# Performance work log

Hardware: AMD Instinct MI355X
Metric: run time of the kernel (lower is better)

The kernel has to match this reference:

```python
import jax, jax.numpy as jnp
import numpy as np

B, S, D_IN, H, NH, L = 8, 1024, 512, 1024, 16, 4
HD = H // NH
SCALE = HD ** -0.5
EPS = 1e-5


def _ln(x, g, b):
    m = jnp.mean(x, axis=-1, keepdims=True)
    v = jnp.mean((x - m) ** 2, axis=-1, keepdims=True)
    return (x - m) * jax.lax.rsqrt(v + EPS) * g + b


def setup_inputs() -> dict:
    key = jax.random.key(0)
    ks = jax.random.split(key, 12)
    s = lambda k, shape, fan: jax.random.normal(k, shape, jnp.float32) * (fan ** -0.5)
    return {
        "x": jax.random.normal(ks[0], (B, S, D_IN), jnp.float32),
        "W_in": s(ks[1], (D_IN, H), D_IN), "b_in": jnp.zeros((H,), jnp.float32),
        "W_qkv": s(ks[2], (L, H, 3 * H), H), "b_qkv": jnp.zeros((L, 3 * H), jnp.float32),
        "W_o": s(ks[3], (L, H, H), H), "b_o": jnp.zeros((L, H), jnp.float32),
        "g1": jnp.ones((L, H), jnp.float32), "be1": jnp.zeros((L, H), jnp.float32),
        "W_out": s(ks[4], (H, H), H), "b_out": jnp.zeros((H,), jnp.float32),
        "g2": jnp.ones((H,), jnp.float32), "be2": jnp.zeros((H,), jnp.float32),
    }


def _attn_layer(x, Wqkv, bqkv, Wo, bo, g, be):
    b, s, h = x.shape
    qkv = (x @ Wqkv + bqkv).reshape(b, s, 3, NH, HD)
    q = qkv[:, :, 0].transpose(0, 2, 1, 3)  # [B,NH,S,HD]
    k = qkv[:, :, 1].transpose(0, 2, 1, 3)
    v = qkv[:, :, 2].transpose(0, 2, 1, 3)
    scores = jnp.einsum("bhqd,bhkd->bhqk", q, k) * SCALE
    w = jax.nn.softmax(scores, axis=-1)  # dropout is identity in eval
    o = jnp.einsum("bhqk,bhkd->bhqd", w, v)
    o = o.transpose(0, 2, 1, 3).reshape(b, s, h)
    return _ln(o @ Wo + bo + x, g, be)


def reference(x, W_in, b_in, W_qkv, b_qkv, W_o, b_o, g1, be1, W_out, b_out, g2, be2):
    h = x @ W_in + b_in
    for i in range(L):
        h = _attn_layer(h, W_qkv[i], b_qkv[i], W_o[i], b_o[i], g1[i], be1[i])
    pooled = jnp.mean(h, axis=1)  # [B,H]
    return _ln(pooled @ W_out + b_out, g2, be2)
```

## Files before the change

kernel.cpp:

```cpp
#include <hip/hip_runtime.h>
#include <stdint.h>

typedef unsigned short u16;
typedef unsigned int   u32;
typedef __attribute__((ext_vector_type(8))) short short8;
typedef __attribute__((ext_vector_type(4))) float f32x4;

#define B_   8
#define S_   1024
#define DIN_ 512
#define H_   1024
#define NH_  16
#define HD_  64
#define L_   4
#define M_   (B_*S_)
#define SCALE_ 0.125f
#define EPS_ 1e-5f

__device__ __forceinline__ u16 f2b(float f) {
  u32 u = __builtin_bit_cast(u32, f);
  u32 r = (u + 0x7fffu + ((u >> 16) & 1u)) >> 16;
  return (u16)r;
}

__device__ __forceinline__ void gll16(const void* g, void* l) {
  __builtin_amdgcn_global_load_lds(
      (const __attribute__((address_space(1))) u32*)(uintptr_t)g,
      (__attribute__((address_space(3))) u32*)(uintptr_t)l,
      16, 0, 0);
}

__global__ void cvt_k(const float* __restrict__ in, u16* __restrict__ out) {
  long i = (long)(blockIdx.x * 256 + threadIdx.x) * 4;
  f32x4 v = *(const f32x4*)&in[i];
  u32 p0 = (u32)f2b(v[0]) | ((u32)f2b(v[1]) << 16);
  u32 p1 = (u32)f2b(v[2]) | ((u32)f2b(v[3]) << 16);
  u32* o = (u32*)&out[i];
  o[0] = p0; o[1] = p1;
}

__global__ __launch_bounds__(256)
void tcvt_k(const float* __restrict__ in0, u16* __restrict__ out0, int R, int C) {
  __shared__ float t[32][33];
  const float* in = in0 + (size_t)blockIdx.z * R * C;
  u16* out = out0 + (size_t)blockIdx.z * R * C;
  int tx = threadIdx.x & 31, ty = threadIdx.x >> 5;
  long r0 = blockIdx.y * 32, c0 = blockIdx.x * 32;
#pragma unroll
  for (int i = 0; i < 4; ++i)
    t[ty + i*8][tx] = in[(r0 + ty + i*8) * (long)C + c0 + tx];
  __syncthreads();
#pragma unroll
  for (int i = 0; i < 4; ++i)
    out[(c0 + ty + i*8) * (long)R + r0 + tx] = f2b(t[tx][ty + i*8]);
}

template<int EPI>
__global__ __launch_bounds__(256, 2)
void gemm_k(const u16* __restrict__ A, const u16* __restrict__ Bt,
            const float* __restrict__ bias,
            float* __restrict__ Cf, u16* __restrict__ Cb,
            const float* __restrict__ Res,
            int Ndim, int K, int scale_cols)
{
  __shared__ u16 As[128 * 32];
  __shared__ u16 Bs[128 * 32];
  const int tid = threadIdx.x;
  const int lane = tid & 63;
  const int wid = tid >> 6;
  const int wr = wid >> 1, wc = wid & 1;
  const int l15 = lane & 15, l4 = lane >> 4;
  const long arow0 = (long)blockIdx.x * 128;
  const long brow0 = (long)blockIdx.y * 128;

  f32x4 acc[4][4] = {};

  const int srow = tid >> 2;
  const int scol = (tid & 3) * 8;
  const u16* ga  = A  + (arow0 + srow) * K + scol;
  const u16* ga1 = ga + 64 * (long)K;
  const u16* gb  = Bt + (brow0 + srow) * K + scol;
  const u16* gb1 = gb + 64 * (long)K;
  u16* lA0 = &As[tid * 8];
  u16* lA1 = &As[2048 + tid * 8];
  u16* lB0 = &Bs[tid * 8];
  u16* lB1 = &Bs[2048 + tid * 8];

  for (int k0 = 0; k0 < K; k0 += 32) {
    gll16(ga + k0, lA0);
    gll16(ga1 + k0, lA1);
    gll16(gb + k0, lB0);
    gll16(gb1 + k0, lB1);
    __syncthreads();
    short8 af[4], bf[4];
#pragma unroll
    for (int m = 0; m < 4; ++m)
      af[m] = *(const short8*)&As[(wr*64 + m*16 + l15) * 32 + l4*8];
#pragma unroll
    for (int n = 0; n < 4; ++n)
      bf[n] = *(const short8*)&Bs[(wc*64 + n*16 + l15) * 32 + l4*8];
#pragma unroll
    for (int m = 0; m < 4; ++m)
#pragma unroll
      for (int n = 0; n < 4; ++n)
        acc[m][n] = __builtin_amdgcn_mfma_f32_16x16x32_bf16(af[m], bf[n], acc[m][n], 0, 0, 0);
    __syncthreads();
  }

  const int crow = wr*64 + l4*4;
  const int ccol = wc*64 + l15;
#pragma unroll
  for (int m = 0; m < 4; ++m) {
#pragma unroll
    for (int n = 0; n < 4; ++n) {
      const int col = (int)brow0 + ccol + n*16;
      const float bv = bias[col];
      const float sc = (EPI == 1 && col < scale_cols) ? SCALE_ : 1.0f;
#pragma unroll
      for (int r = 0; r < 4; ++r) {
        const long row = arow0 + crow + m*16 + r;
        float v = acc[m][n][r] + bv;
        if (EPI == 1) {
          Cb[row * Ndim + col] = f2b(v * sc);
        } else if (EPI == 0) {
          Cf[row * Ndim + col] = v;
          Cb[row * Ndim + col] = f2b(v);
        } else {
          Cf[row * Ndim + col] = v + Res[row * Ndim + col];
        }
      }
    }
  }
}

__global__ __launch_bounds__(256, 3)
void attn_k(const u16* __restrict__ qkv, u16* __restrict__ ob)
{
  __shared__ u16 Ks[2][4096];
  __shared__ u16 Vs[2][4096];
  __shared__ u16 Ps[4][2048];

  const int tid = threadIdx.x, lane = tid & 63, wid = tid >> 6;
  const int l15 = lane & 15, l4 = lane >> 4;

  const int hb = blockIdx.x;
  const int xcd = hb & 7, slot = hb >> 3;
  const int bh = xcd + ((slot >> 3) << 3);
  const int qx = slot & 7;
  const int b = bh >> 4, nh = bh & 15;
  const int q0 = qx * 128 + wid * 32;

  const int RS = 3 * H_;
  const long base = (long)b * S_ * RS;
  const u16* Qg = qkv + base + nh * HD_;
  const u16* Kg = qkv + base + H_ + nh * HD_;
  const u16* Vg = qkv + base + 2 * H_ + nh * HD_;

  short8 qf[2][2];
#pragma unroll
  for (int i = 0; i < 2; ++i)
#pragma unroll
    for (int kf = 0; kf < 2; ++kf)
      qf[i][kf] = *(const short8*)&Qg[(long)(q0 + i*16 + l15) * RS + kf*32 + l4*8];

  float m_[2] = {-1e30f, -1e30f};
  float l_[2] = {0.f, 0.f};
  f32x4 of[2][4] = {};

  const int vd = tid & 63;
  const int vk0 = (tid >> 6) * 8;
  const int vbyt0 = (vd*128 + (tid>>6)*16) ^ ((vd & 7) << 4);
  const int vbyt1 = (vd*128 + ((tid>>6)+4)*16) ^ ((vd & 7) << 4);

  {
#pragma unroll
    for (int i = 0; i < 2; ++i) {
      int c = (i*4 + wid) * 64 + lane;
      int row = c >> 3;
      int sc2 = (lane & 7) ^ (row & 7);
      gll16(Kg + (long)row * RS + sc2*8, (char*)&Ks[0][0] + (size_t)c*16);
    }
    union { u16 u[8]; short8 v; } ta, tb;
#pragma unroll
    for (int j = 0; j < 8; ++j) {
      ta.u[j] = Vg[(long)(vk0 + j) * RS + vd];
      tb.u[j] = Vg[(long)(vk0 + 32 + j) * RS + vd];
    }
    *(short8*)((char*)&Vs[0][0] + vbyt0) = ta.v;
    *(short8*)((char*)&Vs[0][0] + vbyt1) = tb.v;
  }
  __syncthreads();

  for (int t = 0; t < 16; ++t) {
    const int cur = t & 1, nxt = cur ^ 1;
    union { u16 u[8]; short8 v; } ta, tb;
    if (t < 15) {
      const int kv1 = (t + 1) * 64;
#pragma unroll
      for (int i = 0; i < 2; ++i) {
        int c = (i*4 + wid) * 64 + lane;
        int row = c >> 3;
        int sc2 = (lane & 7) ^ (row & 7);
        gll16(Kg + (long)(kv1 + row) * RS + sc2*8, (char*)&Ks[nxt][0] + (size_t)c*16);
      }
#pragma unroll
      for (int j = 0; j < 8; ++j) {
        ta.u[j] = Vg[(long)(kv1 + vk0 + j) * RS + vd];
        tb.u[j] = Vg[(long)(kv1 + vk0 + 32 + j) * RS + vd];
      }
    }

    f32x4 sv[2][4];
#pragma unroll
    for (int i = 0; i < 2; ++i)
#pragma unroll
      for (int f = 0; f < 4; ++f)
        sv[i][f] = (f32x4){0.f, 0.f, 0.f, 0.f};
    __builtin_amdgcn_s_setprio(1);
#pragma unroll
    for (int f = 0; f < 4; ++f) {
#pragma unroll
      for (int kf = 0; kf < 2; ++kf) {
        int krow = f*16 + l15;
        int kbyt = (krow*128 + (kf*32 + l4*8)*2) ^ ((krow & 7) << 4);
        short8 kfrag = *(const short8*)((const char*)&Ks[cur][0] + kbyt);
#pragma unroll
        for (int i = 0; i < 2; ++i)
          sv[i][f] = __builtin_amdgcn_mfma_f32_16x16x32_bf16(kfrag, qf[i][kf], sv[i][f], 0, 0, 0);
      }
    }
    __builtin_amdgcn_s_setprio(0);

#pragma unroll
    for (int i = 0; i < 2; ++i) {
      float tmax = -1e30f;
#pragma unroll
      for (int f = 0; f < 4; ++f)
#pragma unroll
        for (int r = 0; r < 4; ++r) tmax = fmaxf(tmax, sv[i][f][r]);
      tmax = fmaxf(tmax, __shfl_xor(tmax, 16));
      tmax = fmaxf(tmax, __shfl_xor(tmax, 32));
      const float mnew = fmaxf(m_[i], tmax);
      const float corr = __expf(m_[i] - mnew);
      float tsum = 0.f;
#pragma unroll
      for (int f = 0; f < 4; ++f) {
#pragma unroll
        for (int r = 0; r < 4; ++r) {
          float p = __expf(sv[i][f][r] - mnew);
          sv[i][f][r] = p;
          tsum += p;
        }
      }
      tsum += __shfl_xor(tsum, 16);
      tsum += __shfl_xor(tsum, 32);
      l_[i] = l_[i] * corr + tsum;
      m_[i] = mnew;
#pragma unroll
      for (int f = 0; f < 4; ++f) {
        u32 lo = (u32)f2b(sv[i][f][0]) | ((u32)f2b(sv[i][f][1]) << 16);
        u32 hi = (u32)f2b(sv[i][f][2]) | ((u32)f2b(sv[i][f][3]) << 16);
        int prow = i*16 + l15;
        int pbyt = (prow*128 + (f*16 + l4*4)*2) ^ ((prow & 7) << 4);
        u32* dst = (u32*)((char*)&Ps[wid][0] + pbyt);
        dst[0] = lo; dst[1] = hi;
      }
#pragma unroll
      for (int r = 0; r < 4; ++r) {
        float cr = __shfl(corr, (lane & 48) | (l4*4 + r));
#pragma unroll
        for (int nf = 0; nf < 4; ++nf) of[i][nf][r] *= cr;
      }
    }
    asm volatile("s_waitcnt lgkmcnt(0)" ::: "memory");
    __builtin_amdgcn_sched_barrier(0);

    __builtin_amdgcn_s_setprio(1);
#pragma unroll
    for (int kf = 0; kf < 2; ++kf) {
      short8 vf_[4];
#pragma unroll
      for (int nf = 0; nf < 4; ++nf) {
        int vrow = nf*16 + l15;
        int vbyt = (vrow*128 + (kf*32 + l4*8)*2) ^ ((vrow & 7) << 4);
        vf_[nf] = *(const short8*)((const char*)&Vs[cur][0] + vbyt);
      }
#pragma unroll
      for (int i = 0; i < 2; ++i) {
        int prow = i*16 + l15;
        int pbyt = (prow*128 + (kf*32 + l4*8)*2) ^ ((prow & 7) << 4);
        short8 pfrag = *(const short8*)((const char*)&Ps[wid][0] + pbyt);
#pragma unroll
        for (int nf = 0; nf < 4; ++nf)
          of[i][nf] = __builtin_amdgcn_mfma_f32_16x16x32_bf16(pfrag, vf_[nf], of[i][nf], 0, 0, 0);
      }
    }
    __builtin_amdgcn_s_setprio(0);

    if (t < 15) {
      *(short8*)((char*)&Vs[nxt][0] + vbyt0) = ta.v;
      *(short8*)((char*)&Vs[nxt][0] + vbyt1) = tb.v;
      __syncthreads();
    }
  }

#pragma unroll
  for (int i = 0; i < 2; ++i) {
#pragma unroll
    for (int r = 0; r < 4; ++r) {
      float li = __shfl(l_[i], (lane & 48) | (l4*4 + r));
      float inv = 1.0f / li;
      long srow = (long)(b * S_ + q0 + i*16 + l4*4 + r);
#pragma unroll
      for (int nf = 0; nf < 4; ++nf)
        ob[srow * H_ + nh*HD_ + nf*16 + l15] = f2b(of[i][nf][r] * inv);
    }
  }
}

__global__ __launch_bounds__(256)
void ln_k(const float* __restrict__ in, const float* __restrict__ g,
          const float* __restrict__ be, float* __restrict__ outf,
          u16* __restrict__ outb)
{
  const int row = blockIdx.x;
  const int tid = threadIdx.x;
  const float* x = in + (long)row * H_;
  f32x4 v = *(const f32x4*)&x[tid * 4];
  float s  = v[0] + v[1] + v[2] + v[3];
  float ss = v[0]*v[0] + v[1]*v[1] + v[2]*v[2] + v[3]*v[3];
#pragma unroll
  for (int o = 1; o < 64; o <<= 1) {
    s  += __shfl_xor(s, o);
    ss += __shfl_xor(ss, o);
  }
  __shared__ float rs[4], rq[4];
  const int wid = tid >> 6;
  if ((tid & 63) == 0) { rs[wid] = s; rq[wid] = ss; }
  __syncthreads();
  float ts = rs[0] + rs[1] + rs[2] + rs[3];
  float tq = rq[0] + rq[1] + rq[2] + rq[3];
  const float mu = ts * (1.0f / H_);
  const float var = tq * (1.0f / H_) - mu * mu;
  const float rstd = rsqrtf(var + EPS_);
  const long obase = (long)row * H_ + tid * 4;
#pragma unroll
  for (int j = 0; j < 4; ++j) {
    int c = tid * 4 + j;
    float y = (v[j] - mu) * rstd * g[c] + be[c];
    outf[obase + j] = y;
    if (outb) outb[obase + j] = f2b(y);
  }
}

__global__ void pool_k(const float* __restrict__ hf, float* __restrict__ pooled) {
  const int c = blockIdx.x * 256 + threadIdx.x;
  const int b = blockIdx.y;
  const int s0 = blockIdx.z * 128;
  float s = 0.f;
  for (int t = 0; t < 128; ++t) s += hf[((long)(b * S_ + s0 + t)) * H_ + c];
  atomicAdd(&pooled[b * H_ + c], s * (1.0f / S_));
}

__global__ void fgemm_k(const float* __restrict__ pooled, const float* __restrict__ W,
                        const float* __restrict__ bias, float* __restrict__ out) {
  const int n = blockIdx.x * 256 + threadIdx.x;
  const int b = blockIdx.y;
  float s = bias[n];
  for (int k = 0; k < H_; ++k) s += pooled[b * H_ + k] * W[(long)k * H_ + n];
  out[b * H_ + n] = s;
}

extern "C" void kernel_launch(void* const* d_in, const int* in_sizes, int n_in,
                              void* d_out, int out_size, void* d_ws, size_t ws_size,
                              hipStream_t stream) {
  const float* x     = (const float*)d_in[0];
  const float* W_in  = (const float*)d_in[1];
  const float* b_in  = (const float*)d_in[2];
  const float* W_qkv = (const float*)d_in[3];
  const float* b_qkv = (const float*)d_in[4];
  const float* W_o   = (const float*)d_in[5];
  const float* b_o   = (const float*)d_in[6];
  const float* g1    = (const float*)d_in[7];
  const float* be1   = (const float*)d_in[8];
  const float* W_out = (const float*)d_in[9];
  const float* b_out = (const float*)d_in[10];
  const float* g2    = (const float*)d_in[11];
  const float* be2   = (const float*)d_in[12];
  float* outp = (float*)d_out;

  char* ws = (char*)d_ws;
  float* hf    = (float*)(ws + 0);
  u16*   hb    = (u16*)(ws + 33554432);
  u16*   qkvb  = (u16*)(ws + 50331648);
  float* resf  = (float*)(ws + 50331648);
  u16*   ob    = (u16*)(ws + 100663296);
  u16*   xb    = (u16*)(ws + 100663296);
  u16*   WinT  = (u16*)(ws + 117440512);
  u16*   WqkvT = (u16*)(ws + 118489088);
  u16*   WoT   = (u16*)(ws + 143654912);
  float* pooled= (float*)(ws + 152043520);
  float* tmpf  = (float*)(ws + 152076288);

  cvt_k<<<dim3(M_ * DIN_ / 1024), 256, 0, stream>>>(x, xb);
  tcvt_k<<<dim3(H_/32, DIN_/32, 1), 256, 0, stream>>>(W_in, WinT, DIN_, H_);
  tcvt_k<<<dim3(3*H_/32, H_/32, L_), 256, 0, stream>>>(W_qkv, WqkvT, H_, 3*H_);
  tcvt_k<<<dim3(H_/32, H_/32, L_), 256, 0, stream>>>(W_o, WoT, H_, H_);

  gemm_k<0><<<dim3(M_/128, H_/128), 256, 0, stream>>>(xb, WinT, b_in, hf, hb, nullptr, H_, DIN_, 0);

  for (int l = 0; l < L_; ++l) {
    gemm_k<1><<<dim3(M_/128, 3*H_/128), 256, 0, stream>>>(hb, WqkvT + (size_t)l*3*H_*H_,
                                                          b_qkv + l*3*H_, nullptr, qkvb, nullptr,
                                                          3*H_, H_, H_);
    attn_k<<<dim3(S_/128 * B_ * NH_), 256, 0, stream>>>(qkvb, ob);
    gemm_k<2><<<dim3(M_/128, H_/128), 256, 0, stream>>>(ob, WoT + (size_t)l*H_*H_,
                                                        b_o + l*H_, resf, nullptr, hf,
                                                        H_, H_, 0);
    ln_k<<<dim3(M_), 256, 0, stream>>>(resf, g1 + l*H_, be1 + l*H_, hf, hb);
  }

  hipMemsetAsync(pooled, 0, B_ * H_ * sizeof(float), stream);
  pool_k<<<dim3(H_/256, B_, 8), 256, 0, stream>>>(hf, pooled);
  fgemm_k<<<dim3(H_/256, B_), 256, 0, stream>>>(pooled, W_out, b_out, tmpf);
  ln_k<<<dim3(B_), 256, 0, stream>>>(tmpf, g2, be2, outp, nullptr);
}
```

Measured before the change: 1.085 ms.

## Rewrite attention with 32x32 MFMA, register P via permlane swap, 512-thread blocks

The attention kernel switches from 16x16x32 to 32x32x16 bf16 MFMA. The P matrix now stays in registers, rearranged with permlane32_swap and v_cvt_pk_bf16, so the LDS round trip for P goes away. Blocks grow to 512 threads with 8 waves covering 256 queries, so each K/V tile load is shared across more queries. It also adds a lazy max rescale that skips the correction unless the max grows by more than 8, cutting exp and multiply work at some numerical risk and adding warp divergence.

```diff
diff --git a/kernel.cpp b/kernel.cpp
--- a/kernel.cpp
+++ b/kernel.cpp
@@ -5,6 +5,8 @@
 typedef unsigned int   u32;
 typedef __attribute__((ext_vector_type(8))) short short8;
 typedef __attribute__((ext_vector_type(4))) float f32x4;
+typedef __attribute__((ext_vector_type(16))) float f32x16;
+typedef __attribute__((ext_vector_type(2))) unsigned int uint2v;
 
 #define B_   8
 #define S_   1024
@@ -21,6 +23,12 @@
   u32 u = __builtin_bit_cast(u32, f);
   u32 r = (u + 0x7fffu + ((u >> 16) & 1u)) >> 16;
   return (u16)r;
+}
+
+__device__ __forceinline__ u32 cvtpk(float lo, float hi) {
+  u32 r;
+  asm("v_cvt_pk_bf16_f32 %0, %1, %2" : "=v"(r) : "v"(lo), "v"(hi));
+  return r;
 }
 
 __device__ __forceinline__ void gll16(const void* g, void* l) {
@@ -133,22 +141,21 @@
   }
 }
 
-__global__ __launch_bounds__(256, 3)
+__global__ __launch_bounds__(512)
 void attn_k(const u16* __restrict__ qkv, u16* __restrict__ ob)
 {
   __shared__ u16 Ks[2][4096];
   __shared__ u16 Vs[2][4096];
-  __shared__ u16 Ps[4][2048];
 
   const int tid = threadIdx.x, lane = tid & 63, wid = tid >> 6;
-  const int l15 = lane & 15, l4 = lane >> 4;
-
-  const int hb = blockIdx.x;
-  const int xcd = hb & 7, slot = hb >> 3;
-  const int bh = xcd + ((slot >> 3) << 3);
-  const int qx = slot & 7;
+  const int l31 = lane & 31, hi = lane >> 5;
+
+  const int blk = blockIdx.x;
+  const int xcd = blk & 7, slot = blk >> 3;
+  const int bh = xcd + ((slot >> 2) << 3);
+  const int qx = slot & 3;
   const int b = bh >> 4, nh = bh & 15;
-  const int q0 = qx * 128 + wid * 32;
+  const int q0 = qx * 256 + wid * 32;
 
   const int RS = 3 * H_;
   const long base = (long)b * S_ * RS;
@@ -156,165 +163,131 @@
   const u16* Kg = qkv + base + H_ + nh * HD_;
   const u16* Vg = qkv + base + 2 * H_ + nh * HD_;
 
-  short8 qf[2][2];
-#pragma unroll
-  for (int i = 0; i < 2; ++i)
-#pragma unroll
-    for (int kf = 0; kf < 2; ++kf)
-      qf[i][kf] = *(const short8*)&Qg[(long)(q0 + i*16 + l15) * RS + kf*32 + l4*8];
-
-  float m_[2] = {-1e30f, -1e30f};
-  float l_[2] = {0.f, 0.f};
-  f32x4 of[2][4] = {};
-
-  const int vd = tid & 63;
-  const int vk0 = (tid >> 6) * 8;
-  const int vbyt0 = (vd*128 + (tid>>6)*16) ^ ((vd & 7) << 4);
-  const int vbyt1 = (vd*128 + ((tid>>6)+4)*16) ^ ((vd & 7) << 4);
+  short8 qf[4];
+#pragma unroll
+  for (int ks = 0; ks < 4; ++ks)
+    qf[ks] = *(const short8*)&Qg[(long)(q0 + l31) * RS + ks*16 + hi*8];
+
+  float m_ = -1e30f, l_ = 0.f;
+  f32x16 o0 = {}, o1 = {};
+
+  const int krow = tid >> 3, kc = tid & 7;
+  const int ksc = kc ^ (krow & 7);
+  const long kgoff = (long)krow * RS + ksc * 8;
+  const int vd = tid & 63, vch = tid >> 6;
+  const int vbyt = (vd*128 + vch*16) ^ ((vd & 7) << 4);
 
   {
-#pragma unroll
-    for (int i = 0; i < 2; ++i) {
-      int c = (i*4 + wid) * 64 + lane;
-      int row = c >> 3;
-      int sc2 = (lane & 7) ^ (row & 7);
-      gll16(Kg + (long)row * RS + sc2*8, (char*)&Ks[0][0] + (size_t)c*16);
-    }
-    union { u16 u[8]; short8 v; } ta, tb;
-#pragma unroll
-    for (int j = 0; j < 8; ++j) {
-      ta.u[j] = Vg[(long)(vk0 + j) * RS + vd];
-      tb.u[j] = Vg[(long)(vk0 + 32 + j) * RS + vd];
-    }
-    *(short8*)((char*)&Vs[0][0] + vbyt0) = ta.v;
-    *(short8*)((char*)&Vs[0][0] + vbyt1) = tb.v;
+    gll16(Kg + kgoff, (char*)&Ks[0][0] + tid*16);
+    union { u16 u[8]; short8 v; } tv;
+#pragma unroll
+    for (int j = 0; j < 8; ++j)
+      tv.u[j] = Vg[(long)(vch*8 + j) * RS + vd];
+    *(short8*)((char*)&Vs[0][0] + vbyt) = tv.v;
   }
   __syncthreads();
 
   for (int t = 0; t < 16; ++t) {
     const int cur = t & 1, nxt = cur ^ 1;
-    union { u16 u[8]; short8 v; } ta, tb;
+    union { u16 u[8]; short8 v; } ta;
     if (t < 15) {
-      const int kv1 = (t + 1) * 64;
-#pragma unroll
-      for (int i = 0; i < 2; ++i) {
-        int c = (i*4 + wid) * 64 + lane;
-        int row = c >> 3;
-        int sc2 = (lane & 7) ^ (row & 7);
-        gll16(Kg + (long)(kv1 + row) * RS + sc2*8, (char*)&Ks[nxt][0] + (size_t)c*16);
+      const long kv1 = (long)(t + 1) * 64;
+      gll16(Kg + kv1 * RS + kgoff, (char*)&Ks[nxt][0] + tid*16);
+#pragma unroll
+      for (int j = 0; j < 8; ++j)
+        ta.u[j] = Vg[(kv1 + vch*8 + j) * RS + vd];
+    }
+
+    f32x16 s0 = {}, s1 = {};
+    __builtin_amdgcn_s_setprio(1);
+#pragma unroll
+    for (int ks = 0; ks < 4; ++ks) {
+      const int koff = ks*32 + hi*16;
+      const int by0 = (l31*128 + koff) ^ ((l31 & 7) << 4);
+      short8 kf0 = *(const short8*)((const char*)&Ks[cur][0] + by0);
+      s0 = __builtin_amdgcn_mfma_f32_32x32x16_bf16(kf0, qf[ks], s0, 0, 0, 0);
+      const int by1 = ((32 + l31)*128 + koff) ^ ((l31 & 7) << 4);
+      short8 kf1 = *(const short8*)((const char*)&Ks[cur][0] + by1);
+      s1 = __builtin_amdgcn_mfma_f32_32x32x16_bf16(kf1, qf[ks], s1, 0, 0, 0);
+    }
+    __builtin_amdgcn_s_setprio(0);
+
+    float tmax = -1e30f;
+#pragma unroll
+    for (int r = 0; r < 16; ++r) tmax = fmaxf(tmax, fmaxf(s0[r], s1[r]));
+    tmax = fmaxf(tmax, __shfl_xor(tmax, 32));
+    if (!__all(tmax <= m_ + 8.f)) {
+      const float mnew = fmaxf(m_, tmax);
+      const float corr = __expf(m_ - mnew);
+      m_ = mnew; l_ *= corr;
+#pragma unroll
+      for (int r = 0; r < 16; ++r) {
+        float cr = __shfl(corr, (r&3) + 8*(r>>2) + 4*hi);
+        o0[r] *= cr; o1[r] *= cr;
       }
-#pragma unroll
-      for (int j = 0; j < 8; ++j) {
-        ta.u[j] = Vg[(long)(kv1 + vk0 + j) * RS + vd];
-        tb.u[j] = Vg[(long)(kv1 + vk0 + 32 + j) * RS + vd];
-      }
-    }
-
-    f32x4 sv[2][4];
-#pragma unroll
-    for (int i = 0; i < 2; ++i)
-#pragma unroll
-      for (int f = 0; f < 4; ++f)
-        sv[i][f] = (f32x4){0.f, 0.f, 0.f, 0.f};
+    }
+    float sum = 0.f;
+#pragma unroll
+    for (int r = 0; r < 16; ++r) {
+      float p0 = __expf(s0[r] - m_);
+      float p1 = __expf(s1[r] - m_);
+      s0[r] = p0; s1[r] = p1;
+      sum += p0 + p1;
+    }
+    sum += __shfl_xor(sum, 32);
+    l_ += sum;
+
+    short8 pa[4];
+#pragma unroll
+    for (int ks2 = 0; ks2 < 2; ++ks2) {
+      const int r0 = 8 * ks2;
+      u32 A0 = cvtpk(s0[r0+0], s0[r0+1]), A1 = cvtpk(s0[r0+2], s0[r0+3]);
+      u32 B0 = cvtpk(s0[r0+4], s0[r0+5]), B1 = cvtpk(s0[r0+6], s0[r0+7]);
+      uint2v w02 = __builtin_amdgcn_permlane32_swap(A0, B0, false, false);
+      uint2v w13 = __builtin_amdgcn_permlane32_swap(A1, B1, false, false);
+      union { u32 w[4]; short8 v; } u_;
+      u_.w[0] = w02.x; u_.w[1] = w13.x; u_.w[2] = w02.y; u_.w[3] = w13.y;
+      pa[ks2] = u_.v;
+    }
+#pragma unroll
+    for (int ks2 = 0; ks2 < 2; ++ks2) {
+      const int r0 = 8 * ks2;
+      u32 A0 = cvtpk(s1[r0+0], s1[r0+1]), A1 = cvtpk(s1[r0+2], s1[r0+3]);
+      u32 B0 = cvtpk(s1[r0+4], s1[r0+5]), B1 = cvtpk(s1[r0+6], s1[r0+7]);
+      uint2v w02 = __builtin_amdgcn_permlane32_swap(A0, B0, false, false);
+      uint2v w13 = __builtin_amdgcn_permlane32_swap(A1, B1, false, false);
+      union { u32 w[4]; short8 v; } u_;
+      u_.w[0] = w02.x; u_.w[1] = w13.x; u_.w[2] = w02.y; u_.w[3] = w13.y;
+      pa[2 + ks2] = u_.v;
+    }
+
     __builtin_amdgcn_s_setprio(1);
 #pragma unroll
-    for (int f = 0; f < 4; ++f) {
-#pragma unroll
-      for (int kf = 0; kf < 2; ++kf) {
-        int krow = f*16 + l15;
-        int kbyt = (krow*128 + (kf*32 + l4*8)*2) ^ ((krow & 7) << 4);
-        short8 kfrag = *(const short8*)((const char*)&Ks[cur][0] + kbyt);
-#pragma unroll
-        for (int i = 0; i < 2; ++i)
-          sv[i][f] = __builtin_amdgcn_mfma_f32_16x16x32_bf16(kfrag, qf[i][kf], sv[i][f], 0, 0, 0);
-      }
+    for (int ks = 0; ks < 4; ++ks) {
+      const int vb = ks*32 + hi*16;
+      const int by0 = (l31*128 + vb) ^ ((l31 & 7) << 4);
+      short8 v0 = *(const short8*)((const char*)&Vs[cur][0] + by0);
+      o0 = __builtin_amdgcn_mfma_f32_32x32x16_bf16(pa[ks], v0, o0, 0, 0, 0);
+      const int by1 = ((32 + l31)*128 + vb) ^ ((l31 & 7) << 4);
+      short8 v1 = *(const short8*)((const char*)&Vs[cur][0] + by1);
+      o1 = __builtin_amdgcn_mfma_f32_32x32x16_bf16(pa[ks], v1, o1, 0, 0, 0);
     }
     __builtin_amdgcn_s_setprio(0);
 
-#pragma unroll
-    for (int i = 0; i < 2; ++i) {
-      float tmax = -1e30f;
-#pragma unroll
-      for (int f = 0; f < 4; ++f)
-#pragma unroll
-        for (int r = 0; r < 4; ++r) tmax = fmaxf(tmax, sv[i][f][r]);
-      tmax = fmaxf(tmax, __shfl_xor(tmax, 16));
-      tmax = fmaxf(tmax, __shfl_xor(tmax, 32));
-      const float mnew = fmaxf(m_[i], tmax);
-      const float corr = __expf(m_[i] - mnew);
-      float tsum = 0.f;
-#pragma unroll
-      for (int f = 0; f < 4; ++f) {
-#pragma unroll
-        for (int r = 0; r < 4; ++r) {
-          float p = __expf(sv[i][f][r] - mnew);
-          sv[i][f][r] = p;
-          tsum += p;
-        }
-      }
-      tsum += __shfl_xor(tsum, 16);
-      tsum += __shfl_xor(tsum, 32);
-      l_[i] = l_[i] * corr + tsum;
-      m_[i] = mnew;
-#pragma unroll
-      for (int f = 0; f < 4; ++f) {
-        u32 lo = (u32)f2b(sv[i][f][0]) | ((u32)f2b(sv[i][f][1]) << 16);
-        u32 hi = (u32)f2b(sv[i][f][2]) | ((u32)f2b(sv[i][f][3]) << 16);
-        int prow = i*16 + l15;
-        int pbyt = (prow*128 + (f*16 + l4*4)*2) ^ ((prow & 7) << 4);
-        u32* dst = (u32*)((char*)&Ps[wid][0] + pbyt);
-        dst[0] = lo; dst[1] = hi;
-      }
-#pragma unroll
-      for (int r = 0; r < 4; ++r) {
-        float cr = __shfl(corr, (lane & 48) | (l4*4 + r));
-#pragma unroll
-        for (int nf = 0; nf < 4; ++nf) of[i][nf][r] *= cr;
-      }
-    }
-    asm volatile("s_waitcnt lgkmcnt(0)" ::: "memory");
-    __builtin_amdgcn_sched_barrier(0);
-
-    __builtin_amdgcn_s_setprio(1);
-#pragma unroll
-    for (int kf = 0; kf < 2; ++kf) {
-      short8 vf_[4];
-#pragma unroll
-      for (int nf = 0; nf < 4; ++nf) {
-        int vrow = nf*16 + l15;
-        int vbyt = (vrow*128 + (kf*32 + l4*8)*2) ^ ((vrow & 7) << 4);
-        vf_[nf] = *(const short8*)((const char*)&Vs[cur][0] + vbyt);
-      }
-#pragma unroll
-      for (int i = 0; i < 2; ++i) {
-        int prow = i*16 + l15;
-        int pbyt = (prow*128 + (kf*32 + l4*8)*2) ^ ((prow & 7) << 4);
-        short8 pfrag = *(const short8*)((const char*)&Ps[wid][0] + pbyt);
-#pragma unroll
-        for (int nf = 0; nf < 4; ++nf)
-          of[i][nf] = __builtin_amdgcn_mfma_f32_16x16x32_bf16(pfrag, vf_[nf], of[i][nf], 0, 0, 0);
-      }
-    }
-    __builtin_amdgcn_s_setprio(0);
-
     if (t < 15) {
-      *(short8*)((char*)&Vs[nxt][0] + vbyt0) = ta.v;
-      *(short8*)((char*)&Vs[nxt][0] + vbyt1) = tb.v;
+      *(short8*)((char*)&Vs[nxt][0] + vbyt) = ta.v;
       __syncthreads();
     }
   }
 
-#pragma unroll
-  for (int i = 0; i < 2; ++i) {
-#pragma unroll
-    for (int r = 0; r < 4; ++r) {
-      float li = __shfl(l_[i], (lane & 48) | (l4*4 + r));
-      float inv = 1.0f / li;
-      long srow = (long)(b * S_ + q0 + i*16 + l4*4 + r);
-#pragma unroll
-      for (int nf = 0; nf < 4; ++nf)
-        ob[srow * H_ + nh*HD_ + nf*16 + l15] = f2b(of[i][nf][r] * inv);
-    }
+  const float linv = 1.0f / l_;
+#pragma unroll
+  for (int r = 0; r < 16; ++r) {
+    const int rowq = (r&3) + 8*(r>>2) + 4*hi;
+    const float li = __shfl(linv, rowq);
+    const long srow = (long)(b * S_ + q0 + rowq);
+    ob[srow * H_ + nh*HD_ + l31]      = f2b(o0[r] * li);
+    ob[srow * H_ + nh*HD_ + 32 + l31] = f2b(o1[r] * li);
   }
 }
 
@@ -413,7 +386,7 @@
     gemm_k<1><<<dim3(M_/128, 3*H_/128), 256, 0, stream>>>(hb, WqkvT + (size_t)l*3*H_*H_,
                                                           b_qkv + l*3*H_, nullptr, qkvb, nullptr,
                                                           3*H_, H_, H_);
-    attn_k<<<dim3(S_/128 * B_ * NH_), 256, 0, stream>>>(qkvb, ob);
+    attn_k<<<dim3(512), 512, 0, stream>>>(qkvb, ob);
     gemm_k<2><<<dim3(M_/128, H_/128), 256, 0, stream>>>(ob, WoT + (size_t)l*H_*H_,
                                                         b_o + l*H_, resf, nullptr, hf,
                                                         H_, H_, 0);
```

Result: faster. 951.6 us (-12.3%).
